# Kernel optimization log

Hardware: AMD Instinct MI355X
Metric: run time of the kernel (lower is better)

Reference implementation:

```python
import jax, jax.numpy as jnp
import numpy as np

N_NODES = 50000
N_EDGES = 800000
NDIM_IN = 64
EDIM = 64
HID = 152  # size_embedding
NDIM_OUT = 64


def _linear(x, W, b):
    # torch nn.Linear: y = x @ W.T + b
    return jnp.matmul(x, W.T) + b


def _sage_layer(nf, ef, Wm, bm, Wa, ba, src, dst):
    # message: gather src node feats, concat edge feats, linear -> [E,1,F]
    m = _linear(jnp.concatenate([nf[src], ef], axis=2), Wm, bm)
    # mean scatter-reduce to dst nodes (zero for nodes with no in-edges)
    s = jax.ops.segment_sum(m, dst, num_segments=N_NODES)
    deg = jax.ops.segment_sum(jnp.ones((m.shape[0],), m.dtype), dst, num_segments=N_NODES)
    h_neigh = s / jnp.maximum(deg, 1.0)[:, None, None]
    # update: concat self + neighbor agg, linear, relu
    return jax.nn.relu(_linear(jnp.concatenate([nf, h_neigh], axis=2), Wa, ba))


def setup_inputs() -> dict:
    key = jax.random.key(0)
    ks = jax.random.split(key, 16)
    def lin_params(kw, kb, fan_in, fan_out):
        bound = 1.0 / np.sqrt(fan_in)
        W = jax.random.uniform(kw, (fan_out, fan_in), jnp.float32, -bound, bound)
        b = jax.random.uniform(kb, (fan_out,), jnp.float32, -bound, bound)
        return W, b
    nfeats = jax.random.normal(ks[0], (N_NODES, 1, NDIM_IN), jnp.float32)
    efeats = jax.random.normal(ks[1], (N_EDGES, 1, EDIM), jnp.float32)
    src = jax.random.randint(ks[2], (N_EDGES,), 0, N_NODES, jnp.int32)
    dst = jax.random.randint(ks[3], (N_EDGES,), 0, N_NODES, jnp.int32)
    Wm1, bm1 = lin_params(ks[4], ks[5], NDIM_IN + EDIM, HID)
    Wa1, ba1 = lin_params(ks[6], ks[7], NDIM_IN + HID, HID)
    Wm2, bm2 = lin_params(ks[8], ks[9], HID + EDIM, HID)
    Wa2, ba2 = lin_params(ks[10], ks[11], HID + HID, HID)
    Wm3, bm3 = lin_params(ks[12], ks[13], HID + EDIM, NDIM_OUT)
    Wa3, ba3 = lin_params(ks[14], ks[15], HID + NDIM_OUT, NDIM_OUT)
    return {
        "nfeats": nfeats, "efeats": efeats,
        "Wm1": Wm1, "bm1": bm1, "Wa1": Wa1, "ba1": ba1,
        "Wm2": Wm2, "bm2": bm2, "Wa2": Wa2, "ba2": ba2,
        "Wm3": Wm3, "bm3": bm3, "Wa3": Wa3, "ba3": ba3,
        "src": src, "dst": dst,
    }


def reference(nfeats, efeats, Wm1, bm1, Wa1, ba1, Wm2, bm2, Wa2, ba2,
              Wm3, bm3, Wa3, ba3, src, dst):
    # dropout is identity in eval mode
    h = _sage_layer(nfeats, efeats, Wm1, bm1, Wa1, ba1, src, dst)
    h = _sage_layer(h, efeats, Wm2, bm2, Wa2, ba2, src, dst)
    h = _sage_layer(h, efeats, Wm3, bm3, Wa3, ba3, src, dst)
    return h.sum(axis=1)  # [N, ndim_out]
```

## Files before the change

### kernel.cpp

```cpp
#include <hip/hip_runtime.h>


#define NN 50000
#define NE 800000
#define NIN 64
#define EDIM_ 64
#define HID_ 152
#define NOUT 64
#define PADN 50176

__global__ __launch_bounds__(256) void hist_kernel(const int* __restrict__ dst,
                                                   int* __restrict__ ideg) {
    int e = blockIdx.x * 256 + threadIdx.x;
    if (e < NE) atomicAdd(&ideg[dst[e]], 1);
}

__global__ __launch_bounds__(256) void scan1_kernel(const int* __restrict__ in,
                                                    int* __restrict__ out,
                                                    int* __restrict__ bsum) {
    __shared__ int ws[4];
    int t = threadIdx.x;
    int base = blockIdx.x * 1024 + t * 4;
    int a0 = in[base], a1 = in[base + 1], a2 = in[base + 2], a3 = in[base + 3];
    int s = a0 + a1 + a2 + a3;
    int lane = t & 63, wid = t >> 6;
    int v = s;
#pragma unroll
    for (int d = 1; d < 64; d <<= 1) {
        int u = __shfl_up(v, d);
        if (lane >= d) v += u;
    }
    if (lane == 63) ws[wid] = v;
    __syncthreads();
    int wofs = 0;
    if (wid > 0) wofs += ws[0];
    if (wid > 1) wofs += ws[1];
    if (wid > 2) wofs += ws[2];
    int excl = wofs + v - s;
    out[base] = excl;
    out[base + 1] = excl + a0;
    out[base + 2] = excl + a0 + a1;
    out[base + 3] = excl + a0 + a1 + a2;
    if (t == 255) bsum[blockIdx.x] = wofs + v;
}

__global__ __launch_bounds__(64) void scan2_kernel(int* __restrict__ bsum, int nb) {
    int t = threadIdx.x;
    int orig = (t < nb) ? bsum[t] : 0;
    int v = orig;
#pragma unroll
    for (int d = 1; d < 64; d <<= 1) {
        int u = __shfl_up(v, d);
        if (t >= d) v += u;
    }
    if (t < nb) bsum[t] = v - orig;
}

__global__ __launch_bounds__(256) void scan3_kernel(int* __restrict__ out,
                                                    const int* __restrict__ bsum) {
    int base = blockIdx.x * 1024 + threadIdx.x * 4;
    int b = bsum[blockIdx.x];
    out[base] += b; out[base + 1] += b; out[base + 2] += b; out[base + 3] += b;
}

__global__ __launch_bounds__(256) void scatter_edges_kernel(const int* __restrict__ src,
                                                            const int* __restrict__ dst,
                                                            int* __restrict__ cursor,
                                                            int* __restrict__ csr_nf,
                                                            int* __restrict__ csr_ef) {
    int e = blockIdx.x * 256 + threadIdx.x;
    if (e >= NE) return;
    int d = dst[e];
    int pos = atomicAdd(&cursor[d], 1);
    csr_nf[pos] = src[e];
    csr_ef[pos] = e;
}

template <int F>
__global__ __launch_bounds__(256) void agg_kernel(const float* __restrict__ table,
                                                  const int* __restrict__ rows,
                                                  const int* __restrict__ off,
                                                  float* __restrict__ out) {
    constexpr int C = F / 4;
    constexpr int NPW = 64 / C;
    int t = threadIdx.x;
    int lane = t & 63, wid = t >> 6;
    int sub = lane / C;
    int ch = lane - sub * C;
    int n = (blockIdx.x * 4 + wid) * NPW + sub;
    if (sub >= NPW || n >= NN) return;
    int s = off[n], e = off[n + 1];
    float ax0 = 0.f, ax1 = 0.f, ax2 = 0.f, ax3 = 0.f;
    float bx0 = 0.f, bx1 = 0.f, bx2 = 0.f, bx3 = 0.f;
    int i = s;
    for (; i + 1 < e; i += 2) {
        int r0 = rows[i], r1 = rows[i + 1];
        float4 v0 = *(const float4*)(table + (size_t)r0 * F + ch * 4);
        float4 v1 = *(const float4*)(table + (size_t)r1 * F + ch * 4);
        ax0 += v0.x; ax1 += v0.y; ax2 += v0.z; ax3 += v0.w;
        bx0 += v1.x; bx1 += v1.y; bx2 += v1.z; bx3 += v1.w;
    }
    if (i < e) {
        int r0 = rows[i];
        float4 v0 = *(const float4*)(table + (size_t)r0 * F + ch * 4);
        ax0 += v0.x; ax1 += v0.y; ax2 += v0.z; ax3 += v0.w;
    }
    float4 r;
    r.x = ax0 + bx0; r.y = ax1 + bx1; r.z = ax2 + bx2; r.w = ax3 + bx3;
    *(float4*)(out + (size_t)n * F + ch * 4) = r;
}

template <int K1, int K2, int NT, bool MSG>
__global__ __launch_bounds__(256) void gemm_kernel(const float* __restrict__ X1,
                                                   const float* __restrict__ X2,
                                                   const float* __restrict__ W,
                                                   const float* __restrict__ bias,
                                                   const int* __restrict__ off,
                                                   float* __restrict__ out) {
    constexpr int KT = K1 + K2;
    __shared__ float Xs[8][68];
    __shared__ float Ws[8][68];
    const int t = threadIdx.x;
    const int m0 = blockIdx.x * 64;
    const int n0 = blockIdx.y * 64;
    const int lm = t >> 2;
    const int lk = (t & 3) * 2;
    const int tx = t & 15;
    const int ty = t >> 4;
    float acc[4][4] = {};

    const bool xrow_ok = (m0 + lm) < NN;
    const bool wrow_ok = (n0 + lm) < NT;

#pragma unroll
    for (int seg = 0; seg < 2; ++seg) {
        const float* __restrict__ X = seg ? X2 : X1;
        const int K = seg ? K2 : K1;
        const int koff = seg ? K1 : 0;
        for (int k0 = 0; k0 < K; k0 += 8) {
            float2 xv = make_float2(0.f, 0.f);
            if (xrow_ok) xv = *(const float2*)(X + (size_t)(m0 + lm) * K + k0 + lk);
            float2 wv = make_float2(0.f, 0.f);
            if (wrow_ok) wv = *(const float2*)(W + (size_t)(n0 + lm) * KT + koff + k0 + lk);
            __syncthreads();
            Xs[lk][lm] = xv.x; Xs[lk + 1][lm] = xv.y;
            Ws[lk][lm] = wv.x; Ws[lk + 1][lm] = wv.y;
            __syncthreads();
#pragma unroll
            for (int k = 0; k < 8; ++k) {
                float a0 = Xs[k][ty * 4 + 0], a1 = Xs[k][ty * 4 + 1];
                float a2 = Xs[k][ty * 4 + 2], a3 = Xs[k][ty * 4 + 3];
                float b0 = Ws[k][tx * 4 + 0], b1 = Ws[k][tx * 4 + 1];
                float b2 = Ws[k][tx * 4 + 2], b3 = Ws[k][tx * 4 + 3];
                acc[0][0] += a0 * b0; acc[0][1] += a0 * b1; acc[0][2] += a0 * b2; acc[0][3] += a0 * b3;
                acc[1][0] += a1 * b0; acc[1][1] += a1 * b1; acc[1][2] += a1 * b2; acc[1][3] += a1 * b3;
                acc[2][0] += a2 * b0; acc[2][1] += a2 * b1; acc[2][2] += a2 * b2; acc[2][3] += a2 * b3;
                acc[3][0] += a3 * b0; acc[3][1] += a3 * b1; acc[3][2] += a3 * b2; acc[3][3] += a3 * b3;
            }
        }
    }

    const int o0 = n0 + tx * 4;
    if (o0 >= NT) return;
    float b0 = bias[o0], b1 = bias[o0 + 1], b2 = bias[o0 + 2], b3 = bias[o0 + 3];
#pragma unroll
    for (int i = 0; i < 4; ++i) {
        int n = m0 + ty * 4 + i;
        if (n >= NN) break;
        float4 r;
        if (MSG) {
            float d = (float)(off[n + 1] - off[n]);
            float inv = 1.0f / fmaxf(d, 1.0f);
            r.x = (acc[i][0] + d * b0) * inv;
            r.y = (acc[i][1] + d * b1) * inv;
            r.z = (acc[i][2] + d * b2) * inv;
            r.w = (acc[i][3] + d * b3) * inv;
        } else {
            r.x = fmaxf(acc[i][0] + b0, 0.0f);
            r.y = fmaxf(acc[i][1] + b1, 0.0f);
            r.z = fmaxf(acc[i][2] + b2, 0.0f);
            r.w = fmaxf(acc[i][3] + b3, 0.0f);
        }
        *(float4*)(out + (size_t)n * NT + o0) = r;
    }
}

extern "C" void kernel_launch(void* const* d_in, const int* in_sizes, int n_in,
                              void* d_out, int out_size, void* d_ws, size_t ws_size,
                              hipStream_t stream) {
    const float* nfeats = (const float*)d_in[0];
    const float* efeats = (const float*)d_in[1];
    const float* Wm1 = (const float*)d_in[2];
    const float* bm1 = (const float*)d_in[3];
    const float* Wa1 = (const float*)d_in[4];
    const float* ba1 = (const float*)d_in[5];
    const float* Wm2 = (const float*)d_in[6];
    const float* bm2 = (const float*)d_in[7];
    const float* Wa2 = (const float*)d_in[8];
    const float* ba2 = (const float*)d_in[9];
    const float* Wm3 = (const float*)d_in[10];
    const float* bm3 = (const float*)d_in[11];
    const float* Wa3 = (const float*)d_in[12];
    const float* ba3 = (const float*)d_in[13];
    const int* src = (const int*)d_in[14];
    const int* dst = (const int*)d_in[15];
    float* out = (float*)d_out;

    int* iws = (int*)d_ws;
    int* ideg   = iws;
    int* off    = iws + PADN;
    int* cursor = iws + 2 * PADN;
    int* csr_nf = iws + 3 * PADN;
    int* csr_ef = csr_nf + NE;
    float* B = (float*)(csr_ef + NE);
    float* P = B + 3200000;
    float* Q = P + 7600000;
    float* R = Q + 7600000;

    const int BLK = 256;
    auto cdiv = [](long long a, long long b) { return (int)((a + b - 1) / b); };
    dim3 g152(cdiv(NN, 64), cdiv(152, 64));
    dim3 g64(cdiv(NN, 64), 1);
    const int NB = PADN / 1024;

    hipMemsetAsync(ideg, 0, (size_t)PADN * 4, stream);
    hist_kernel<<<cdiv(NE, BLK), BLK, 0, stream>>>(dst, ideg);
    scan1_kernel<<<NB, 256, 0, stream>>>(ideg, off, cursor);
    scan2_kernel<<<1, 64, 0, stream>>>(cursor, NB);
    scan3_kernel<<<NB, 256, 0, stream>>>(off, cursor);
    hipMemcpyAsync(cursor, off, (size_t)NN * 4, hipMemcpyDeviceToDevice, stream);
    scatter_edges_kernel<<<cdiv(NE, BLK), BLK, 0, stream>>>(src, dst, cursor, csr_nf, csr_ef);

    agg_kernel<EDIM_><<<cdiv(NN, 16), BLK, 0, stream>>>(efeats, csr_ef, off, B);

    agg_kernel<NIN><<<cdiv(NN, 16), BLK, 0, stream>>>(nfeats, csr_nf, off, P);
    gemm_kernel<NIN, EDIM_, HID_, true><<<g152, BLK, 0, stream>>>(P, B, Wm1, bm1, off, Q);
    gemm_kernel<NIN, HID_, HID_, false><<<g152, BLK, 0, stream>>>(nfeats, Q, Wa1, ba1, off, R);

    agg_kernel<HID_><<<cdiv(NN, 4), BLK, 0, stream>>>(R, csr_nf, off, P);
    gemm_kernel<HID_, EDIM_, HID_, true><<<g152, BLK, 0, stream>>>(P, B, Wm2, bm2, off, Q);
    gemm_kernel<HID_, HID_, HID_, false><<<g152, BLK, 0, stream>>>(R, Q, Wa2, ba2, off, P);

    agg_kernel<HID_><<<cdiv(NN, 4), BLK, 0, stream>>>(P, csr_nf, off, Q);
    gemm_kernel<HID_, EDIM_, NOUT, true><<<g64, BLK, 0, stream>>>(Q, B, Wm3, bm3, off, R);
    gemm_kernel<HID_, NOUT, NOUT, false><<<g64, BLK, 0, stream>>>(P, R, Wa3, ba3, off, out);
}
```

Before: 937.1 us.

## Enlarge GEMM tile to 128x64 with 16-wide K slabs and register prefetch

Reworks the fused linear GEMM kernel so each block computes a 128-row by 64-column tile, with each thread holding an 8x4 accumulator, and walks K in slabs of 16 instead of 8. The two input segments are merged into a single K loop, and the next slab is prefetched into registers during compute so shared-memory stores and barriers happen once per slab. LDS reads become float4-vectorised. This aims to raise arithmetic intensity and cut barrier and global-load overhead, at the cost of more registers (possibly lower occupancy) and fewer blocks in the grid.

```diff
diff --git a/kernel.cpp b/kernel.cpp
--- a/kernel.cpp
+++ b/kernel.cpp
@@ -118,68 +118,102 @@
                                                    const int* __restrict__ off,
                                                    float* __restrict__ out) {
     constexpr int KT = K1 + K2;
-    __shared__ float Xs[8][68];
-    __shared__ float Ws[8][68];
+    constexpr int NKS = (KT + 15) / 16;
+    __shared__ float Xs[16][132];
+    __shared__ float Ws[16][68];
+
     const int t = threadIdx.x;
-    const int m0 = blockIdx.x * 64;
+    const int m0 = blockIdx.x * 128;
     const int n0 = blockIdx.y * 64;
-    const int lm = t >> 2;
-    const int lk = (t & 3) * 2;
+
+    const int xm = t >> 1;
+    const int xh = (t & 1) * 8;
+    const int wn = t >> 2;
+    const int wc = (t & 3) * 4;
+
     const int tx = t & 15;
     const int ty = t >> 4;
-    float acc[4][4] = {};
-
-    const bool xrow_ok = (m0 + lm) < NN;
-    const bool wrow_ok = (n0 + lm) < NT;
-
-#pragma unroll
-    for (int seg = 0; seg < 2; ++seg) {
-        const float* __restrict__ X = seg ? X2 : X1;
-        const int K = seg ? K2 : K1;
-        const int koff = seg ? K1 : 0;
-        for (int k0 = 0; k0 < K; k0 += 8) {
-            float2 xv = make_float2(0.f, 0.f);
-            if (xrow_ok) xv = *(const float2*)(X + (size_t)(m0 + lm) * K + k0 + lk);
-            float2 wv = make_float2(0.f, 0.f);
-            if (wrow_ok) wv = *(const float2*)(W + (size_t)(n0 + lm) * KT + koff + k0 + lk);
+
+    const int xrow = m0 + xm;
+    const bool xok = xrow < NN;
+    const bool wok = (n0 + wn) < NT;
+    const float* __restrict__ xrp1 = X1 + (size_t)xrow * K1;
+    const float* __restrict__ xrp2 = X2 + (size_t)xrow * K2;
+    const float* __restrict__ wrp  = W + (size_t)(n0 + wn) * KT;
+
+    float acc[8][4] = {};
+    float4 rx0, rx1, rw;
+
+    auto loadT = [&](int k0) {
+        const int kv = k0 + xh;
+        rx0 = make_float4(0.f, 0.f, 0.f, 0.f);
+        rx1 = rx0;
+        if (xok && kv < KT) {
+            const float* p = (kv < K1) ? (xrp1 + kv) : (xrp2 + (kv - K1));
+            rx0 = *(const float4*)p;
+            rx1 = *(const float4*)(p + 4);
+        }
+        rw = make_float4(0.f, 0.f, 0.f, 0.f);
+        const int kw = k0 + wc;
+        if (wok && kw < KT) rw = *(const float4*)(wrp + kw);
+    };
+    auto storeT = [&]() {
+        Xs[xh + 0][xm] = rx0.x; Xs[xh + 1][xm] = rx0.y;
+        Xs[xh + 2][xm] = rx0.z; Xs[xh + 3][xm] = rx0.w;
+        Xs[xh + 4][xm] = rx1.x; Xs[xh + 5][xm] = rx1.y;
+        Xs[xh + 6][xm] = rx1.z; Xs[xh + 7][xm] = rx1.w;
+        Ws[wc + 0][wn] = rw.x;  Ws[wc + 1][wn] = rw.y;
+        Ws[wc + 2][wn] = rw.z;  Ws[wc + 3][wn] = rw.w;
+    };
+
+    loadT(0);
+    storeT();
+    __syncthreads();
+
+    for (int s = 0; s < NKS; ++s) {
+        const bool more = (s + 1 < NKS);
+        if (more) loadT((s + 1) * 16);
+#pragma unroll
+        for (int k = 0; k < 16; ++k) {
+            const float4 xa = *(const float4*)&Xs[k][ty * 8];
+            const float4 xb = *(const float4*)&Xs[k][ty * 8 + 4];
+            const float4 wv = *(const float4*)&Ws[k][tx * 4];
+            const float xv[8] = {xa.x, xa.y, xa.z, xa.w, xb.x, xb.y, xb.z, xb.w};
+#pragma unroll
+            for (int i = 0; i < 8; ++i) {
+                acc[i][0] += xv[i] * wv.x;
+                acc[i][1] += xv[i] * wv.y;
+                acc[i][2] += xv[i] * wv.z;
+                acc[i][3] += xv[i] * wv.w;
+            }
+        }
+        if (more) {
             __syncthreads();
-            Xs[lk][lm] = xv.x; Xs[lk + 1][lm] = xv.y;
-            Ws[lk][lm] = wv.x; Ws[lk + 1][lm] = wv.y;
+            storeT();
             __syncthreads();
-#pragma unroll
-            for (int k = 0; k < 8; ++k) {
-                float a0 = Xs[k][ty * 4 + 0], a1 = Xs[k][ty * 4 + 1];
-                float a2 = Xs[k][ty * 4 + 2], a3 = Xs[k][ty * 4 + 3];
-                float b0 = Ws[k][tx * 4 + 0], b1 = Ws[k][tx * 4 + 1];
-                float b2 = Ws[k][tx * 4 + 2], b3 = Ws[k][tx * 4 + 3];
-                acc[0][0] += a0 * b0; acc[0][1] += a0 * b1; acc[0][2] += a0 * b2; acc[0][3] += a0 * b3;
-                acc[1][0] += a1 * b0; acc[1][1] += a1 * b1; acc[1][2] += a1 * b2; acc[1][3] += a1 * b3;
-                acc[2][0] += a2 * b0; acc[2][1] += a2 * b1; acc[2][2] += a2 * b2; acc[2][3] += a2 * b3;
-                acc[3][0] += a3 * b0; acc[3][1] += a3 * b1; acc[3][2] += a3 * b2; acc[3][3] += a3 * b3;
-            }
         }
     }
 
     const int o0 = n0 + tx * 4;
     if (o0 >= NT) return;
-    float b0 = bias[o0], b1 = bias[o0 + 1], b2 = bias[o0 + 2], b3 = bias[o0 + 3];
-#pragma unroll
-    for (int i = 0; i < 4; ++i) {
-        int n = m0 + ty * 4 + i;
+    const float4 bv = *(const float4*)(bias + o0);
+#pragma unroll
+    for (int i = 0; i < 8; ++i) {
+        const int n = m0 + ty * 8 + i;
         if (n >= NN) break;
         float4 r;
         if (MSG) {
             float d = (float)(off[n + 1] - off[n]);
             float inv = 1.0f / fmaxf(d, 1.0f);
-            r.x = (acc[i][0] + d * b0) * inv;
-            r.y = (acc[i][1] + d * b1) * inv;
-            r.z = (acc[i][2] + d * b2) * inv;
-            r.w = (acc[i][3] + d * b3) * inv;
+            r.x = (acc[i][0] + d * bv.x) * inv;
+            r.y = (acc[i][1] + d * bv.y) * inv;
+            r.z = (acc[i][2] + d * bv.z) * inv;
+            r.w = (acc[i][3] + d * bv.w) * inv;
         } else {
-            r.x = fmaxf(acc[i][0] + b0, 0.0f);
-            r.y = fmaxf(acc[i][1] + b1, 0.0f);
-            r.z = fmaxf(acc[i][2] + b2, 0.0f);
-            r.w = fmaxf(acc[i][3] + b3, 0.0f);
+            r.x = fmaxf(acc[i][0] + bv.x, 0.0f);
+            r.y = fmaxf(acc[i][1] + bv.y, 0.0f);
+            r.z = fmaxf(acc[i][2] + bv.z, 0.0f);
+            r.w = fmaxf(acc[i][3] + bv.w, 0.0f);
         }
         *(float4*)(out + (size_t)n * NT + o0) = r;
     }
@@ -219,8 +253,8 @@
 
     const int BLK = 256;
     auto cdiv = [](long long a, long long b) { return (int)((a + b - 1) / b); };
-    dim3 g152(cdiv(NN, 64), cdiv(152, 64));
-    dim3 g64(cdiv(NN, 64), 1);
+    dim3 g152(cdiv(NN, 128), cdiv(152, 64));
+    dim3 g64(cdiv(NN, 128), 1);
     const int NB = PADN / 1024;
 
     hipMemsetAsync(ideg, 0, (size_t)PADN * 4, stream);
```

Measured after the change: 1.001 ms. 6.8% more time.
